# Optimization experiments

Measured on AMD Instinct MI355X. Metric: run time of the kernel, lower is better.

## Reference

```python
import jax, jax.numpy as jnp
import numpy as np

D_MODEL = 1024
NUM_HEADS = 16
D_FF = 4096
NEG_INF = -1e9


def _linear_params(key, d_in, d_out):
    kw, kb = jax.random.split(key)
    bound = 1.0 / np.sqrt(d_in)
    W = jax.random.uniform(kw, (d_in, d_out), jnp.float32, -bound, bound)
    b = jax.random.uniform(kb, (d_out,), jnp.float32, -bound, bound)
    return W, b


def setup_inputs() -> dict:
    key = jax.random.key(0)
    ks = jax.random.split(key, 8)
    B, S = 2, 2048
    x = jax.random.normal(ks[0], (B, S, D_MODEL), jnp.float32)
    # causal mask: 1 = attend, 0 = masked
    mask = jnp.tril(jnp.ones((S, S), jnp.bool_))[None, :, :]
    Wq, bq = _linear_params(ks[1], D_MODEL, D_MODEL)
    Wk, bk = _linear_params(ks[2], D_MODEL, D_MODEL)
    Wv, bv = _linear_params(ks[3], D_MODEL, D_MODEL)
    Wo, bo = _linear_params(ks[4], D_MODEL, D_MODEL)
    W1, b1 = _linear_params(ks[5], D_MODEL, D_FF)
    W2, b2 = _linear_params(ks[6], D_FF, D_MODEL)
    ln1_g = jnp.ones((D_MODEL,), jnp.float32)
    ln1_b = jnp.zeros((D_MODEL,), jnp.float32)
    ln2_g = jnp.ones((D_MODEL,), jnp.float32)
    ln2_b = jnp.zeros((D_MODEL,), jnp.float32)
    return {"x": x, "mask": mask,
            "Wq": Wq, "bq": bq, "Wk": Wk, "bk": bk, "Wv": Wv, "bv": bv,
            "Wo": Wo, "bo": bo, "W1": W1, "b1": b1, "W2": W2, "b2": b2,
            "ln1_g": ln1_g, "ln1_b": ln1_b, "ln2_g": ln2_g, "ln2_b": ln2_b}


def layer_norm(x, g, b, eps=1e-5):
    mu = jnp.mean(x, axis=-1, keepdims=True)
    var = jnp.mean(jnp.square(x - mu), axis=-1, keepdims=True)
    return (x - mu) * jax.lax.rsqrt(var + eps) * g + b


def attention(xn, mask, Wq, bq, Wk, bk, Wv, bv, Wo, bo):
    B, S, D = xn.shape
    H, dk = NUM_HEADS, D // NUM_HEADS
    q = (xn @ Wq + bq).reshape(B, S, H, dk).transpose(0, 2, 1, 3)  # [B,H,S,dk]
    k = (xn @ Wk + bk).reshape(B, S, H, dk).transpose(0, 2, 1, 3)
    v = (xn @ Wv + bv).reshape(B, S, H, dk).transpose(0, 2, 1, 3)
    scores = jnp.einsum("bhsd,bhtd->bhst", q, k) / jnp.sqrt(jnp.float32(dk))
    scores = jnp.where(mask[:, None, :, :], scores, NEG_INF)
    attn = jax.nn.softmax(scores, axis=-1)
    out = jnp.einsum("bhst,bhtd->bhsd", attn, v)  # [B,H,S,dk]
    out = out.transpose(0, 2, 1, 3).reshape(B, S, D)
    return out @ Wo + bo


def reference(x, mask, Wq, bq, Wk, bk, Wv, bv, Wo, bo, W1, b1, W2, b2,
              ln1_g, ln1_b, ln2_g, ln2_b):
    # pre-norm MHA + residual (dropout = identity at eval)
    h = x + attention(layer_norm(x, ln1_g, ln1_b), mask,
                      Wq, bq, Wk, bk, Wv, bv, Wo, bo)
    # pre-norm FFN + residual
    ff = jax.nn.relu(layer_norm(h, ln2_g, ln2_b) @ W1 + b1) @ W2 + b2
    return h + ff
```

## Files before the change

### kernel.cpp

```cpp
#include <hip/hip_runtime.h>

typedef unsigned short u16;
typedef __attribute__((ext_vector_type(8))) short    s16x8;
typedef __attribute__((ext_vector_type(8))) unsigned short u16x8;
typedef __attribute__((ext_vector_type(4))) float    f32x4;

typedef __attribute__((address_space(1))) const void gvoid_c;
typedef __attribute__((address_space(3))) void       lvoid;

__device__ __forceinline__ float b2f(u16 x) {
    return __builtin_bit_cast(float, (unsigned)x << 16);
}
__device__ __forceinline__ u16 f2bf(float f) {
    unsigned u = __builtin_bit_cast(unsigned, f);
    return (u16)((u + 0x7FFFu + ((u >> 16) & 1u)) >> 16);
}
__device__ __forceinline__ void gld16(const void* g, void* l) {
    __builtin_amdgcn_global_load_lds((gvoid_c*)g, (lvoid*)l, 16, 0, 0);
}

__global__ __launch_bounds__(256) void transpose_f2b(
    const float* __restrict__ in, u16* __restrict__ out, int R, int C)
{
    __shared__ u16 tile[32][33];
    int tx = threadIdx.x & 31, ty = threadIdx.x >> 5;
    int c0 = blockIdx.x * 32, r0 = blockIdx.y * 32;
#pragma unroll
    for (int i = 0; i < 32; i += 8)
        tile[ty + i][tx] = f2bf(in[(size_t)(r0 + ty + i) * C + c0 + tx]);
    __syncthreads();
#pragma unroll
    for (int i = 0; i < 32; i += 8)
        out[(size_t)(c0 + ty + i) * R + r0 + tx] = tile[tx][ty + i];
}

__global__ void concat3(const float* a, const float* b, const float* c, float* o) {
    int i = blockIdx.x * blockDim.x + threadIdx.x;
    o[i] = (i < 1024) ? a[i] : (i < 2048 ? b[i - 1024] : c[i - 2048]);
}

__global__ __launch_bounds__(256) void ln_k(
    const float* __restrict__ in, const float* __restrict__ gg,
    const float* __restrict__ bb, u16* __restrict__ out)
{
    const int D = 1024;
    int row  = blockIdx.x * 4 + (threadIdx.x >> 6);
    int lane = threadIdx.x & 63;
    const float* ip = in + (size_t)row * D;
    float v[16];
#pragma unroll
    for (int cc = 0; cc < 4; cc++) {
        f32x4 t = *(const f32x4*)(ip + cc * 256 + lane * 4);
#pragma unroll
        for (int i = 0; i < 4; i++) v[cc * 4 + i] = t[i];
    }
    float s1 = 0.f, s2 = 0.f;
#pragma unroll
    for (int i = 0; i < 16; i++) { s1 += v[i]; s2 += v[i] * v[i]; }
#pragma unroll
    for (int m = 1; m < 64; m <<= 1) { s1 += __shfl_xor(s1, m); s2 += __shfl_xor(s2, m); }
    float mu   = s1 * (1.f / 1024.f);
    float var  = s2 * (1.f / 1024.f) - mu * mu;
    float rstd = rsqrtf(var + 1e-5f);
#pragma unroll
    for (int cc = 0; cc < 4; cc++) {
        int e = cc * 256 + lane * 4;
        f32x4 gv = *(const f32x4*)(gg + e);
        f32x4 bv = *(const f32x4*)(bb + e);
        u16 o[4];
#pragma unroll
        for (int i = 0; i < 4; i++)
            o[i] = f2bf((v[cc * 4 + i] - mu) * rstd * gv[i] + bv[i]);
        *(__attribute__((ext_vector_type(4))) unsigned short*)(out + (size_t)row * D + e) =
            (__attribute__((ext_vector_type(4))) unsigned short){o[0], o[1], o[2], o[3]};
    }
}

__global__ __launch_bounds__(256) void ffn2_init(
    const float* __restrict__ h, const float* __restrict__ b2,
    float* __restrict__ out)
{
    int i = blockIdx.x * 256 + threadIdx.x;
    f32x4 hv = ((const f32x4*)h)[i];
    f32x4 bv = ((const f32x4*)b2)[i & 255];
    ((f32x4*)out)[i] = hv + bv;
}

template <int BN, int RES, bool RELU, bool OUTF32, bool ATOMIC>
__global__ __launch_bounds__(256) void gemm2(
    const u16* __restrict__ A, const u16* __restrict__ Bt,
    const float* __restrict__ bias, const float* __restrict__ res,
    void* __restrict__ out, int M, int N, int K, int KC)
{
    constexpr int NFR = BN / 32;
    __shared__ u16 As[2][4096];
    __shared__ u16 Bs[2][BN * 32];
    int tid = threadIdx.x, wave = tid >> 6, lane = tid & 63;
    int g = lane >> 4, c = lane & 15;
    int wm = wave >> 1, wn = wave & 1;
    int m0 = blockIdx.y * 128, n0 = blockIdx.x * BN;
    int kst = blockIdx.z * KC;

    f32x4 acc[4][NFR];
#pragma unroll
    for (int m = 0; m < 4; m++)
#pragma unroll
        for (int n = 0; n < NFR; n++) acc[m][n] = (f32x4){0, 0, 0, 0};

    int ch0 = wave * 128 + lane, ch1 = ch0 + 64;
    const u16* Ag0 = A + (size_t)(m0 + (ch0 >> 2)) * K + kst + (ch0 & 3) * 8;
    const u16* Ag1 = A + (size_t)(m0 + (ch1 >> 2)) * K + kst + (ch1 & 3) * 8;
    const u16* Bg0;
    const u16* Bg1 = nullptr;
    if constexpr (BN == 128) {
        Bg0 = Bt + (size_t)(n0 + (ch0 >> 2)) * K + kst + (ch0 & 3) * 8;
        Bg1 = Bt + (size_t)(n0 + (ch1 >> 2)) * K + kst + (ch1 & 3) * 8;
    } else {
        int chb = wave * 64 + lane;
        Bg0 = Bt + (size_t)(n0 + (chb >> 2)) * K + kst + (chb & 3) * 8;
    }

    auto stage = [&](int buf, int kk) {
        gld16(Ag0 + kk, &As[buf][wave * 1024]);
        gld16(Ag1 + kk, &As[buf][wave * 1024 + 512]);
        if constexpr (BN == 128) {
            gld16(Bg0 + kk, &Bs[buf][wave * 1024]);
            gld16(Bg1 + kk, &Bs[buf][wave * 1024 + 512]);
        } else {
            gld16(Bg0 + kk, &Bs[buf][wave * 512]);
        }
    };

    int nt = KC / 32;
    stage(0, 0);
    __syncthreads();
    int cur = 0;
    for (int t = 0; t < nt; t++) {
        if (t + 1 < nt) stage(cur ^ 1, (t + 1) * 32);
        s16x8 af[4], bfr[NFR];
#pragma unroll
        for (int m = 0; m < 4; m++)
            af[m] = *(const s16x8*)&As[cur][(wm * 64 + m * 16 + c) * 32 + g * 8];
#pragma unroll
        for (int n = 0; n < NFR; n++)
            bfr[n] = *(const s16x8*)&Bs[cur][(wn * (BN / 2) + n * 16 + c) * 32 + g * 8];
#pragma unroll
        for (int m = 0; m < 4; m++)
#pragma unroll
            for (int n = 0; n < NFR; n++)
                acc[m][n] = __builtin_amdgcn_mfma_f32_16x16x32_bf16(af[m], bfr[n], acc[m][n], 0, 0, 0);
        __syncthreads();
        cur ^= 1;
    }

#pragma unroll
    for (int n = 0; n < NFR; n++) {
        int col = n0 + wn * (BN / 2) + n * 16 + c;
        float bb = 0.f;
        if constexpr (!ATOMIC) bb = bias[col];
#pragma unroll
        for (int m = 0; m < 4; m++) {
#pragma unroll
            for (int j = 0; j < 4; j++) {
                int row = m0 + wm * 64 + m * 16 + g * 4 + j;
                float v = acc[m][n][j] + bb;
                if constexpr (RES == 2) v += res[(size_t)row * N + col];
                if constexpr (RELU) v = fmaxf(v, 0.f);
                if constexpr (ATOMIC)
                    __hip_atomic_fetch_add(&((float*)out)[(size_t)row * N + col], v,
                                           __ATOMIC_RELAXED, __HIP_MEMORY_SCOPE_AGENT);
                else if constexpr (OUTF32)
                    ((float*)out)[(size_t)row * N + col] = v;
                else
                    ((u16*)out)[(size_t)row * N + col] = f2bf(v);
            }
        }
    }
}

__global__ __launch_bounds__(256) void v_transpose(
    const u16* __restrict__ qkv, u16* __restrict__ vt)
{
    const int S = 2048, NC = 3072;
    __shared__ u16 tile[64][72];
    int st = blockIdx.x, bh = blockIdx.y, b = bh >> 4, h = bh & 15;
    int tid = threadIdx.x;
    int i = tid >> 3, cb8 = (tid & 7) * 8;
    const u16* src = qkv + (size_t)(b * S + st * 64) * NC + 2048 + h * 64;
    u16x8 a0 = *(const u16x8*)(src + (size_t)i * NC + cb8);
    u16x8 a1 = *(const u16x8*)(src + (size_t)(i + 32) * NC + cb8);
    *(u16x8*)&tile[i][cb8]      = a0;
    *(u16x8*)&tile[i + 32][cb8] = a1;
    __syncthreads();
    int d = tid >> 3, e8 = (tid & 7) * 8;
    int m = (d & 7) * 8;
#pragma unroll
    for (int rr = 0; rr < 2; rr++) {
        int r = d + rr * 32;
        u16x8 o;
#pragma unroll
        for (int j = 0; j < 8; j++) o[j] = tile[(e8 ^ m) + j][r];
        *(u16x8*)(vt + ((size_t)bh * 64 + r) * 2048 + st * 64 + e8) = o;
    }
}

__global__ __launch_bounds__(256) void attn_fwd2(
    const u16* __restrict__ qkv, const u16* __restrict__ vt,
    u16* __restrict__ o)
{
    const int S = 2048, NC = 3072;
    __shared__ u16 Ks[4096];
    __shared__ u16 Vs[4096];
    __shared__ u16 Plds[4][16][72];
    int qp = blockIdx.x, bh = blockIdx.y, b = bh >> 4, h = bh & 15;
    int tid = threadIdx.x, wave = tid >> 6, lane = tid & 63;
    int g = lane >> 4, c = lane & 15;
    int sr = tid >> 3, scb8 = (tid & 7) * 8;
    int mS = (sr & 7) * 8;
    int mR = (c & 7) * 8;

    const u16* kbase = qkv + (size_t)b * S * NC + 1024 + h * 64;
    const u16* vbase = vt + (size_t)bh * 64 * 2048;

#pragma unroll 1
    for (int ph = 0; ph < 2; ph++) {
        int qt = ph ? qp : 31 - qp;
        int q0 = qt * 64 + wave * 16;
        const u16* qptr = qkv + (size_t)(b * S + q0 + c) * NC + h * 64;
        s16x8 qf0 = *(const s16x8*)(qptr + g * 8);
        s16x8 qf1 = *(const s16x8*)(qptr + 32 + g * 8);

        float mr[4], lr[4];
        f32x4 acc[4];
#pragma unroll
        for (int j = 0; j < 4; j++) { mr[j] = -1e30f; lr[j] = 0.f; }
#pragma unroll
        for (int n = 0; n < 4; n++) acc[n] = (f32x4){0, 0, 0, 0};

        int ntiles = qt + 1;
        for (int t = 0; t < ntiles; t++) {
            int t0 = t * 64;
            __syncthreads();
            gld16(kbase + (size_t)(t0 + sr)      * NC + (scb8 ^ mS), &Ks[wave * 512]);
            gld16(kbase + (size_t)(t0 + sr + 32) * NC + (scb8 ^ mS), &Ks[2048 + wave * 512]);
            gld16(vbase + (size_t)sr        * 2048 + t0 + scb8, &Vs[wave * 512]);
            gld16(vbase + (size_t)(sr + 32) * 2048 + t0 + scb8, &Vs[2048 + wave * 512]);
            __syncthreads();

            f32x4 s[4];
#pragma unroll
            for (int kt = 0; kt < 4; kt++) {
                int r = kt * 16 + c;
                s16x8 kf0 = *(const s16x8*)&Ks[r * 64 + ((g * 8) ^ mR)];
                s16x8 kf1 = *(const s16x8*)&Ks[r * 64 + ((32 + g * 8) ^ mR)];
                f32x4 sv = (f32x4){0, 0, 0, 0};
                sv = __builtin_amdgcn_mfma_f32_16x16x32_bf16(qf0, kf0, sv, 0, 0, 0);
                sv = __builtin_amdgcn_mfma_f32_16x16x32_bf16(qf1, kf1, sv, 0, 0, 0);
                s[kt] = sv;
            }
#pragma unroll
            for (int kt = 0; kt < 4; kt++) {
                int kcol = t0 + kt * 16 + c;
#pragma unroll
                for (int j = 0; j < 4; j++) {
                    int qrow = q0 + g * 4 + j;
                    s[kt][j] = (kcol <= qrow) ? s[kt][j] * 0.125f : -1e30f;
                }
            }
#pragma unroll
            for (int j = 0; j < 4; j++) {
                float tm = fmaxf(fmaxf(s[0][j], s[1][j]), fmaxf(s[2][j], s[3][j]));
#pragma unroll
                for (int m = 1; m < 16; m <<= 1) tm = fmaxf(tm, __shfl_xor(tm, m));
                float mnew = fmaxf(mr[j], tm);
                float corr = __expf(mr[j] - mnew);
                float rs = 0.f;
#pragma unroll
                for (int kt = 0; kt < 4; kt++) { float p = __expf(s[kt][j] - mnew); s[kt][j] = p; rs += p; }
#pragma unroll
                for (int m = 1; m < 16; m <<= 1) rs += __shfl_xor(rs, m);
                lr[j] = lr[j] * corr + rs;
                mr[j] = mnew;
#pragma unroll
                for (int n = 0; n < 4; n++) acc[n][j] *= corr;
            }
#pragma unroll
            for (int kt = 0; kt < 4; kt++)
#pragma unroll
                for (int j = 0; j < 4; j++)
                    Plds[wave][g * 4 + j][kt * 16 + c] = f2bf(s[kt][j]);
            s16x8 pa0 = *(const s16x8*)&Plds[wave][c][g * 8];
            s16x8 pa1 = *(const s16x8*)&Plds[wave][c][32 + g * 8];
#pragma unroll
            for (int n = 0; n < 4; n++) {
                int r = n * 16 + c;
                s16x8 vb0 = *(const s16x8*)&Vs[r * 64 + ((g * 8) ^ mR)];
                s16x8 vb1 = *(const s16x8*)&Vs[r * 64 + ((32 + g * 8) ^ mR)];
                acc[n] = __builtin_amdgcn_mfma_f32_16x16x32_bf16(pa0, vb0, acc[n], 0, 0, 0);
                acc[n] = __builtin_amdgcn_mfma_f32_16x16x32_bf16(pa1, vb1, acc[n], 0, 0, 0);
            }
        }
#pragma unroll
        for (int j = 0; j < 4; j++) {
            float inv = 1.f / lr[j];
            size_t rbase = (size_t)(b * S + q0 + g * 4 + j) * 1024 + h * 64;
#pragma unroll
            for (int n = 0; n < 4; n++)
                o[rbase + n * 16 + c] = f2bf(acc[n][j] * inv);
        }
    }
}

extern "C" void kernel_launch(void* const* d_in, const int* in_sizes, int n_in,
                              void* d_out, int out_size, void* d_ws, size_t ws_size,
                              hipStream_t stream)
{
    const float* x    = (const float*)d_in[0];
    const float* Wq   = (const float*)d_in[2];  const float* bq = (const float*)d_in[3];
    const float* Wk   = (const float*)d_in[4];  const float* bk = (const float*)d_in[5];
    const float* Wv   = (const float*)d_in[6];  const float* bv = (const float*)d_in[7];
    const float* Wo   = (const float*)d_in[8];  const float* bo = (const float*)d_in[9];
    const float* W1   = (const float*)d_in[10]; const float* b1 = (const float*)d_in[11];
    const float* W2   = (const float*)d_in[12]; const float* b2 = (const float*)d_in[13];
    const float* ln1g = (const float*)d_in[14]; const float* ln1b = (const float*)d_in[15];
    const float* ln2g = (const float*)d_in[16]; const float* ln2b = (const float*)d_in[17];

    unsigned char* ws = (unsigned char*)d_ws;
    u16*   Wqkv_t = (u16*)(ws + 0);
    u16*   Wo_t   = (u16*)(ws + 6291456);
    u16*   W1_t   = (u16*)(ws + 8388608);
    u16*   W2_t   = (u16*)(ws + 16777216);
    float* bqkv   = (float*)(ws + 25165824);
    u16*   lnbuf  = (u16*)(ws + 25178112);
    u16*   qkvbuf = (u16*)(ws + 33566720);
    u16*   attnb  = (u16*)(ws + 58732544);
    u16*   f1buf  = (u16*)(ws + 33566720);
    float* hbuf   = (float*)(ws + 67121152);
    u16*   vtbuf  = (u16*)(ws + 67121152);

    transpose_f2b<<<dim3(32, 32), 256, 0, stream>>>(Wq, Wqkv_t,               1024, 1024);
    transpose_f2b<<<dim3(32, 32), 256, 0, stream>>>(Wk, Wqkv_t + 1024 * 1024, 1024, 1024);
    transpose_f2b<<<dim3(32, 32), 256, 0, stream>>>(Wv, Wqkv_t + 2048 * 1024, 1024, 1024);
    transpose_f2b<<<dim3(32, 32), 256, 0, stream>>>(Wo, Wo_t,                 1024, 1024);
    transpose_f2b<<<dim3(128, 32), 256, 0, stream>>>(W1, W1_t,                1024, 4096);
    transpose_f2b<<<dim3(32, 128), 256, 0, stream>>>(W2, W2_t,                4096, 1024);
    concat3<<<12, 256, 0, stream>>>(bq, bk, bv, bqkv);

    ln_k<<<1024, 256, 0, stream>>>(x, ln1g, ln1b, lnbuf);
    gemm2<128, 0, false, false, false><<<dim3(24, 32, 1), 256, 0, stream>>>(
        lnbuf, Wqkv_t, bqkv, nullptr, qkvbuf, 4096, 3072, 1024, 1024);
    v_transpose<<<dim3(32, 32), 256, 0, stream>>>(qkvbuf, vtbuf);
    attn_fwd2<<<dim3(16, 32), 256, 0, stream>>>(qkvbuf, vtbuf, attnb);

    gemm2<64, 2, false, true, false><<<dim3(16, 32, 1), 256, 0, stream>>>(
        attnb, Wo_t, bo, x, hbuf, 4096, 1024, 1024, 1024);

    ln_k<<<1024, 256, 0, stream>>>(hbuf, ln2g, ln2b, lnbuf);
    gemm2<128, 0, true, false, false><<<dim3(32, 32, 1), 256, 0, stream>>>(
        lnbuf, W1_t, b1, nullptr, f1buf, 4096, 4096, 1024, 1024);
    ffn2_init<<<4096, 256, 0, stream>>>(hbuf, b2, (float*)d_out);
    gemm2<128, 0, false, true, true><<<dim3(8, 32, 4), 256, 0, stream>>>(
        f1buf, W2_t, b2, nullptr, d_out, 4096, 1024, 4096, 1024);
}
```

Measured before the change: 445.3 us.

## Double-buffer attention KV, swizzle GEMM tiles, drop split-K atomics, fuse weight transposes

Several changes at once. The six weight-transpose launches merge into one kernel. GEMM workgroup IDs are remapped with an XCD-aware swizzle, and the MFMA blocks are wrapped in s_setprio. The FFN2 split-K atomic GEMM and its init kernel are replaced by a plain BN=64 GEMM that fuses the bias and residual. The attention kernel now double-buffers its K/V tiles in LDS so the next tile's loads overlap compute, removing one barrier per iteration. The changes aim to cut launch overhead, atomic traffic and load stalls, at the cost of more LDS in attention and less parallelism in FFN2 with the long K loop.

```diff
diff --git a/kernel.cpp b/kernel.cpp
--- a/kernel.cpp
+++ b/kernel.cpp
@@ -19,19 +19,38 @@
     __builtin_amdgcn_global_load_lds((gvoid_c*)g, (lvoid*)l, 16, 0, 0);
 }
 
-__global__ __launch_bounds__(256) void transpose_f2b(
-    const float* __restrict__ in, u16* __restrict__ out, int R, int C)
+__global__ __launch_bounds__(256) void transpose_all(
+    const float* __restrict__ Wq, const float* __restrict__ Wk,
+    const float* __restrict__ Wv, const float* __restrict__ Wo,
+    const float* __restrict__ W1, const float* __restrict__ W2,
+    u16* __restrict__ Wqkv_t, u16* __restrict__ Wo_t,
+    u16* __restrict__ W1_t, u16* __restrict__ W2_t)
 {
     __shared__ u16 tile[32][33];
+    int id = blockIdx.x;
+    const float* src; u16* dst; int R, C, bx, by;
+    if (id < 4096) {
+        int m = id >> 10, r = id & 1023;
+        bx = r & 31; by = r >> 5; R = 1024; C = 1024;
+        src = (m == 0) ? Wq : (m == 1) ? Wk : (m == 2) ? Wv : Wo;
+        dst = (m == 0) ? Wqkv_t : (m == 1) ? Wqkv_t + 1024 * 1024
+            : (m == 2) ? Wqkv_t + 2048 * 1024 : Wo_t;
+    } else if (id < 8192) {
+        int r = id - 4096; bx = r & 127; by = r >> 7; R = 1024; C = 4096;
+        src = W1; dst = W1_t;
+    } else {
+        int r = id - 8192; bx = r & 31; by = r >> 5; R = 4096; C = 1024;
+        src = W2; dst = W2_t;
+    }
     int tx = threadIdx.x & 31, ty = threadIdx.x >> 5;
-    int c0 = blockIdx.x * 32, r0 = blockIdx.y * 32;
+    int c0 = bx * 32, r0 = by * 32;
 #pragma unroll
     for (int i = 0; i < 32; i += 8)
-        tile[ty + i][tx] = f2bf(in[(size_t)(r0 + ty + i) * C + c0 + tx]);
+        tile[ty + i][tx] = f2bf(src[(size_t)(r0 + ty + i) * C + c0 + tx]);
     __syncthreads();
 #pragma unroll
     for (int i = 0; i < 32; i += 8)
-        out[(size_t)(c0 + ty + i) * R + r0 + tx] = tile[tx][ty + i];
+        dst[(size_t)(c0 + ty + i) * R + r0 + tx] = tile[tx][ty + i];
 }
 
 __global__ void concat3(const float* a, const float* b, const float* c, float* o) {
@@ -76,21 +95,11 @@
     }
 }
 
-__global__ __launch_bounds__(256) void ffn2_init(
-    const float* __restrict__ h, const float* __restrict__ b2,
-    float* __restrict__ out)
-{
-    int i = blockIdx.x * 256 + threadIdx.x;
-    f32x4 hv = ((const f32x4*)h)[i];
-    f32x4 bv = ((const f32x4*)b2)[i & 255];
-    ((f32x4*)out)[i] = hv + bv;
-}
-
-template <int BN, int RES, bool RELU, bool OUTF32, bool ATOMIC>
+template <int BN, int RES, bool RELU, bool OUTF32>
 __global__ __launch_bounds__(256) void gemm2(
     const u16* __restrict__ A, const u16* __restrict__ Bt,
     const float* __restrict__ bias, const float* __restrict__ res,
-    void* __restrict__ out, int M, int N, int K, int KC)
+    void* __restrict__ out, int M, int N, int K)
 {
     constexpr int NFR = BN / 32;
     __shared__ u16 As[2][4096];
@@ -98,8 +107,11 @@
     int tid = threadIdx.x, wave = tid >> 6, lane = tid & 63;
     int g = lane >> 4, c = lane & 15;
     int wm = wave >> 1, wn = wave & 1;
-    int m0 = blockIdx.y * 128, n0 = blockIdx.x * BN;
-    int kst = blockIdx.z * KC;
+
+    int gx = gridDim.x, nwg = gx * gridDim.y;
+    int id = blockIdx.y * gx + blockIdx.x;
+    int swz = (id & 7) * (nwg >> 3) + (id >> 3);
+    int m0 = (swz / gx) * 128, n0 = (swz % gx) * BN;
 
     f32x4 acc[4][NFR];
 #pragma unroll
@@ -108,16 +120,16 @@
         for (int n = 0; n < NFR; n++) acc[m][n] = (f32x4){0, 0, 0, 0};
 
     int ch0 = wave * 128 + lane, ch1 = ch0 + 64;
-    const u16* Ag0 = A + (size_t)(m0 + (ch0 >> 2)) * K + kst + (ch0 & 3) * 8;
-    const u16* Ag1 = A + (size_t)(m0 + (ch1 >> 2)) * K + kst + (ch1 & 3) * 8;
+    const u16* Ag0 = A + (size_t)(m0 + (ch0 >> 2)) * K + (ch0 & 3) * 8;
+    const u16* Ag1 = A + (size_t)(m0 + (ch1 >> 2)) * K + (ch1 & 3) * 8;
     const u16* Bg0;
     const u16* Bg1 = nullptr;
     if constexpr (BN == 128) {
-        Bg0 = Bt + (size_t)(n0 + (ch0 >> 2)) * K + kst + (ch0 & 3) * 8;
-        Bg1 = Bt + (size_t)(n0 + (ch1 >> 2)) * K + kst + (ch1 & 3) * 8;
+        Bg0 = Bt + (size_t)(n0 + (ch0 >> 2)) * K + (ch0 & 3) * 8;
+        Bg1 = Bt + (size_t)(n0 + (ch1 >> 2)) * K + (ch1 & 3) * 8;
     } else {
         int chb = wave * 64 + lane;
-        Bg0 = Bt + (size_t)(n0 + (chb >> 2)) * K + kst + (chb & 3) * 8;
+        Bg0 = Bt + (size_t)(n0 + (chb >> 2)) * K + (chb & 3) * 8;
     }
 
     auto stage = [&](int buf, int kk) {
@@ -131,7 +143,7 @@
         }
     };
 
-    int nt = KC / 32;
+    int nt = K / 32;
     stage(0, 0);
     __syncthreads();
     int cur = 0;
@@ -144,11 +156,13 @@
 #pragma unroll
         for (int n = 0; n < NFR; n++)
             bfr[n] = *(const s16x8*)&Bs[cur][(wn * (BN / 2) + n * 16 + c) * 32 + g * 8];
+        __builtin_amdgcn_s_setprio(1);
 #pragma unroll
         for (int m = 0; m < 4; m++)
 #pragma unroll
             for (int n = 0; n < NFR; n++)
                 acc[m][n] = __builtin_amdgcn_mfma_f32_16x16x32_bf16(af[m], bfr[n], acc[m][n], 0, 0, 0);
+        __builtin_amdgcn_s_setprio(0);
         __syncthreads();
         cur ^= 1;
     }
@@ -156,8 +170,7 @@
 #pragma unroll
     for (int n = 0; n < NFR; n++) {
         int col = n0 + wn * (BN / 2) + n * 16 + c;
-        float bb = 0.f;
-        if constexpr (!ATOMIC) bb = bias[col];
+        float bb = bias[col];
 #pragma unroll
         for (int m = 0; m < 4; m++) {
 #pragma unroll
@@ -166,13 +179,8 @@
                 float v = acc[m][n][j] + bb;
                 if constexpr (RES == 2) v += res[(size_t)row * N + col];
                 if constexpr (RELU) v = fmaxf(v, 0.f);
-                if constexpr (ATOMIC)
-                    __hip_atomic_fetch_add(&((float*)out)[(size_t)row * N + col], v,
-                                           __ATOMIC_RELAXED, __HIP_MEMORY_SCOPE_AGENT);
-                else if constexpr (OUTF32)
-                    ((float*)out)[(size_t)row * N + col] = v;
-                else
-                    ((u16*)out)[(size_t)row * N + col] = f2bf(v);
+                if constexpr (OUTF32) ((float*)out)[(size_t)row * N + col] = v;
+                else                  ((u16*)out)[(size_t)row * N + col] = f2bf(v);
             }
         }
     }
@@ -204,13 +212,13 @@
     }
 }
 
-__global__ __launch_bounds__(256) void attn_fwd2(
+__global__ __launch_bounds__(256) void attn_fwd3(
     const u16* __restrict__ qkv, const u16* __restrict__ vt,
     u16* __restrict__ o)
 {
     const int S = 2048, NC = 3072;
-    __shared__ u16 Ks[4096];
-    __shared__ u16 Vs[4096];
+    __shared__ u16 Ks[2][4096];
+    __shared__ u16 Vs[2][4096];
     __shared__ u16 Plds[4][16][72];
     int qp = blockIdx.x, bh = blockIdx.y, b = bh >> 4, h = bh & 15;
     int tid = threadIdx.x, wave = tid >> 6, lane = tid & 63;
@@ -222,6 +230,13 @@
     const u16* kbase = qkv + (size_t)b * S * NC + 1024 + h * 64;
     const u16* vbase = vt + (size_t)bh * 64 * 2048;
 
+    auto stageKV = [&](int buf, int t0) {
+        gld16(kbase + (size_t)(t0 + sr)      * NC + (scb8 ^ mS), &Ks[buf][wave * 512]);
+        gld16(kbase + (size_t)(t0 + sr + 32) * NC + (scb8 ^ mS), &Ks[buf][2048 + wave * 512]);
+        gld16(vbase + (size_t)sr        * 2048 + t0 + scb8, &Vs[buf][wave * 512]);
+        gld16(vbase + (size_t)(sr + 32) * 2048 + t0 + scb8, &Vs[buf][2048 + wave * 512]);
+    };
+
 #pragma unroll 1
     for (int ph = 0; ph < 2; ph++) {
         int qt = ph ? qp : 31 - qp;
@@ -238,26 +253,27 @@
         for (int n = 0; n < 4; n++) acc[n] = (f32x4){0, 0, 0, 0};
 
         int ntiles = qt + 1;
+        __syncthreads();
+        stageKV(0, 0);
+        __syncthreads();
+        int cur = 0;
         for (int t = 0; t < ntiles; t++) {
-            int t0 = t * 64;
-            __syncthreads();
-            gld16(kbase + (size_t)(t0 + sr)      * NC + (scb8 ^ mS), &Ks[wave * 512]);
-            gld16(kbase + (size_t)(t0 + sr + 32) * NC + (scb8 ^ mS), &Ks[2048 + wave * 512]);
-            gld16(vbase + (size_t)sr        * 2048 + t0 + scb8, &Vs[wave * 512]);
-            gld16(vbase + (size_t)(sr + 32) * 2048 + t0 + scb8, &Vs[2048 + wave * 512]);
-            __syncthreads();
+            if (t + 1 < ntiles) stageKV(cur ^ 1, (t + 1) * 64);
 
             f32x4 s[4];
+            __builtin_amdgcn_s_setprio(1);
 #pragma unroll
             for (int kt = 0; kt < 4; kt++) {
                 int r = kt * 16 + c;
-                s16x8 kf0 = *(const s16x8*)&Ks[r * 64 + ((g * 8) ^ mR)];
-                s16x8 kf1 = *(const s16x8*)&Ks[r * 64 + ((32 + g * 8) ^ mR)];
+                s16x8 kf0 = *(const s16x8*)&Ks[cur][r * 64 + ((g * 8) ^ mR)];
+                s16x8 kf1 = *(const s16x8*)&Ks[cur][r * 64 + ((32 + g * 8) ^ mR)];
                 f32x4 sv = (f32x4){0, 0, 0, 0};
                 sv = __builtin_amdgcn_mfma_f32_16x16x32_bf16(qf0, kf0, sv, 0, 0, 0);
                 sv = __builtin_amdgcn_mfma_f32_16x16x32_bf16(qf1, kf1, sv, 0, 0, 0);
                 s[kt] = sv;
             }
+            __builtin_amdgcn_s_setprio(0);
+            int t0 = t * 64;
 #pragma unroll
             for (int kt = 0; kt < 4; kt++) {
                 int kcol = t0 + kt * 16 + c;
@@ -291,14 +307,18 @@
                     Plds[wave][g * 4 + j][kt * 16 + c] = f2bf(s[kt][j]);
             s16x8 pa0 = *(const s16x8*)&Plds[wave][c][g * 8];
             s16x8 pa1 = *(const s16x8*)&Plds[wave][c][32 + g * 8];
+            __builtin_amdgcn_s_setprio(1);
 #pragma unroll
             for (int n = 0; n < 4; n++) {
                 int r = n * 16 + c;
-                s16x8 vb0 = *(const s16x8*)&Vs[r * 64 + ((g * 8) ^ mR)];
-                s16x8 vb1 = *(const s16x8*)&Vs[r * 64 + ((32 + g * 8) ^ mR)];
+                s16x8 vb0 = *(const s16x8*)&Vs[cur][r * 64 + ((g * 8) ^ mR)];
+                s16x8 vb1 = *(const s16x8*)&Vs[cur][r * 64 + ((32 + g * 8) ^ mR)];
                 acc[n] = __builtin_amdgcn_mfma_f32_16x16x32_bf16(pa0, vb0, acc[n], 0, 0, 0);
                 acc[n] = __builtin_amdgcn_mfma_f32_16x16x32_bf16(pa1, vb1, acc[n], 0, 0, 0);
             }
+            __builtin_amdgcn_s_setprio(0);
+            __syncthreads();
+            cur ^= 1;
         }
 #pragma unroll
         for (int j = 0; j < 4; j++) {
@@ -338,27 +358,22 @@
     float* hbuf   = (float*)(ws + 67121152);
     u16*   vtbuf  = (u16*)(ws + 67121152);
 
-    transpose_f2b<<<dim3(32, 32), 256, 0, stream>>>(Wq, Wqkv_t,               1024, 1024);
-    transpose_f2b<<<dim3(32, 32), 256, 0, stream>>>(Wk, Wqkv_t + 1024 * 1024, 1024, 1024);
-    transpose_f2b<<<dim3(32, 32), 256, 0, stream>>>(Wv, Wqkv_t + 2048 * 1024, 1024, 1024);
-    transpose_f2b<<<dim3(32, 32), 256, 0, stream>>>(Wo, Wo_t,                 1024, 1024);
-    transpose_f2b<<<dim3(128, 32), 256, 0, stream>>>(W1, W1_t,                1024, 4096);
-    transpose_f2b<<<dim3(32, 128), 256, 0, stream>>>(W2, W2_t,                4096, 1024);
+    transpose_all<<<12288, 256, 0, stream>>>(Wq, Wk, Wv, Wo, W1, W2,
+                                             Wqkv_t, Wo_t, W1_t, W2_t);
     concat3<<<12, 256, 0, stream>>>(bq, bk, bv, bqkv);
 
     ln_k<<<1024, 256, 0, stream>>>(x, ln1g, ln1b, lnbuf);
-    gemm2<128, 0, false, false, false><<<dim3(24, 32, 1), 256, 0, stream>>>(
-        lnbuf, Wqkv_t, bqkv, nullptr, qkvbuf, 4096, 3072, 1024, 1024);
+    gemm2<128, 0, false, false><<<dim3(24, 32), 256, 0, stream>>>(
+        lnbuf, Wqkv_t, bqkv, nullptr, qkvbuf, 4096, 3072, 1024);
     v_transpose<<<dim3(32, 32), 256, 0, stream>>>(qkvbuf, vtbuf);
-    attn_fwd2<<<dim3(16, 32), 256, 0, stream>>>(qkvbuf, vtbuf, attnb);
-
-    gemm2<64, 2, false, true, false><<<dim3(16, 32, 1), 256, 0, stream>>>(
-        attnb, Wo_t, bo, x, hbuf, 4096, 1024, 1024, 1024);
+    attn_fwd3<<<dim3(16, 32), 256, 0, stream>>>(qkvbuf, vtbuf, attnb);
+
+    gemm2<64, 2, false, true><<<dim3(16, 32), 256, 0, stream>>>(
+        attnb, Wo_t, bo, x, hbuf, 4096, 1024, 1024);
 
     ln_k<<<1024, 256, 0, stream>>>(hbuf, ln2g, ln2b, lnbuf);
-    gemm2<128, 0, true, false, false><<<dim3(32, 32, 1), 256, 0, stream>>>(
-        lnbuf, W1_t, b1, nullptr, f1buf, 4096, 4096, 1024, 1024);
-    ffn2_init<<<4096, 256, 0, stream>>>(hbuf, b2, (float*)d_out);
-    gemm2<128, 0, false, true, true><<<dim3(8, 32, 4), 256, 0, stream>>>(
-        f1buf, W2_t, b2, nullptr, d_out, 4096, 1024, 4096, 1024);
-}
+    gemm2<128, 0, true, false><<<dim3(32, 32), 256, 0, stream>>>(
+        lnbuf, W1_t, b1, nullptr, f1buf, 4096, 4096, 1024);
+    gemm2<64, 2, false, true><<<dim3(16, 32), 256, 0, stream>>>(
+        f1buf, W2_t, b2, hbuf, (float*)d_out, 4096, 1024, 4096);
+}
```

Result: faster. 412.6 us (-7.3%).
